# Performance work log

Hardware: AMD Instinct MI355X
Metric: run time of the kernel (lower is better)

The kernel has to match this reference:

```python
import jax, jax.numpy as jnp
import numpy as np

N_NODES = 30000
N_EDGES = 120000
WIDTH = 32
KER_IN = 6
KER_HID = WIDTH // 4  # 8
DEPTH = 4


def setup_inputs() -> dict:
    key = jax.random.key(0)
    ks = jax.random.split(key, 12)
    x = jax.random.normal(ks[0], (N_NODES, 1), dtype=jnp.float32)
    edge_index = jax.random.randint(ks[1], (2, N_EDGES), 0, N_NODES, dtype=jnp.int64)
    edge_attr = jax.random.uniform(ks[2], (N_EDGES, KER_IN), dtype=jnp.float32)
    # fc1: in_width=1 -> width
    fc1_w = jax.random.normal(ks[3], (1, WIDTH), dtype=jnp.float32) * 0.5
    fc1_b = jnp.zeros((WIDTH,), dtype=jnp.float32)
    # kernel MLP: ker_in -> width//4 -> width*width (per-edge weight matrix)
    k_w1 = jax.random.normal(ks[4], (KER_IN, KER_HID), dtype=jnp.float32) * (1.0 / np.sqrt(KER_IN))
    k_b1 = jnp.zeros((KER_HID,), dtype=jnp.float32)
    k_w2 = jax.random.normal(ks[5], (KER_HID, WIDTH * WIDTH), dtype=jnp.float32) * (1.0 / np.sqrt(KER_HID))
    k_b2 = jnp.zeros((WIDTH * WIDTH,), dtype=jnp.float32)
    # NNConv root weight and bias
    root = jax.random.normal(ks[6], (WIDTH, WIDTH), dtype=jnp.float32) * (1.0 / np.sqrt(WIDTH))
    conv_bias = jnp.zeros((WIDTH,), dtype=jnp.float32)
    # fc2: width -> 1
    fc2_w = jax.random.normal(ks[7], (WIDTH, 1), dtype=jnp.float32) * (1.0 / np.sqrt(WIDTH))
    fc2_b = jnp.zeros((1,), dtype=jnp.float32)
    return {"x": x, "edge_index": edge_index, "edge_attr": edge_attr,
            "fc1_w": fc1_w, "fc1_b": fc1_b,
            "k_w1": k_w1, "k_b1": k_b1, "k_w2": k_w2, "k_b2": k_b2,
            "root": root, "conv_bias": conv_bias,
            "fc2_w": fc2_w, "fc2_b": fc2_b}


def _nnconv(x, src, dst, We, root, bias):
    # x: [N, W]; We: [E, W, W] per-edge weight from kernel MLP
    msg = jnp.einsum('ei,eio->eo', x[src], We)            # gather + per-edge matmul
    agg = jax.ops.segment_sum(msg, dst, num_segments=N_NODES)
    cnt = jax.ops.segment_sum(jnp.ones((msg.shape[0],), msg.dtype), dst, num_segments=N_NODES)
    agg = agg / jnp.maximum(cnt, 1.0)[:, None]            # scatter-mean
    return agg + x @ root + bias


def reference(x, edge_index, edge_attr, fc1_w, fc1_b, k_w1, k_b1, k_w2, k_b2, root, conv_bias, fc2_w, fc2_b):
    src, dst = edge_index[0], edge_index[1]
    h = x @ fc1_w + fc1_b                                 # [N, W]
    # kernel MLP on edge_attr -> per-edge [W, W] weight (edge_attr is fixed, so compute once)
    kh = jax.nn.relu(edge_attr @ k_w1 + k_b1)
    We = (kh @ k_w2 + k_b2).reshape(-1, WIDTH, WIDTH)     # [E, W, W]
    for _ in range(DEPTH):
        h = jax.nn.relu(_nnconv(h, src, dst, We, root, conv_bias))
    return h @ fc2_w + fc2_b                              # [N, 1]
```

## Files before the change

### kernel.cpp

```cpp
#include <hip/hip_runtime.h>

#define NN 30000
#define NE 120000
#define TPB 256
#define SB 118
#define NW 1875

typedef __attribute__((ext_vector_type(8))) __bf16 bf16x8;
typedef __attribute__((ext_vector_type(4))) float f32x4;

union B8 { bf16x8 b; unsigned short u[8]; uint4 q; };

__device__ __forceinline__ float blo(unsigned u) { return __uint_as_float(u << 16); }
__device__ __forceinline__ float bhi(unsigned u) { return __uint_as_float(u & 0xffff0000u); }

__device__ __forceinline__ unsigned short f2b(float f) {
  unsigned u = __float_as_uint(f);
  return (unsigned short)((u + 0x7fff + ((u >> 16) & 1)) >> 16);
}

__device__ __forceinline__ void pack_wb(int f, const float* kw2, const float* kb2,
                                        const float* root, uint4* Wb) {
  int ct = f >> 6, l = f & 63;
  int j = ct * 16 + (l & 15);
  int k = j >> 5, o = j & 31;
  int i0 = (l >> 4) * 8;
  B8 w;
#pragma unroll
  for (int ii = 0; ii < 8; ii++) {
    int i = i0 + ii;
    float v;
    if (k < 8) v = kw2[k * 1024 + i * 32 + o];
    else if (k == 8) v = kb2[i * 32 + o];
    else v = root[i * 32 + o];
    w.u[ii] = f2b(v);
  }
  Wb[f] = w.q;
}

__global__ void k_init(int* __restrict__ cnt, const float* __restrict__ kw2,
                       const float* __restrict__ kb2, const float* __restrict__ root,
                       uint4* __restrict__ Wb) {
  int bid = blockIdx.x;
  if (bid < SB) {
    int n = bid * TPB + threadIdx.x;
    if (n < NN) cnt[n] = 0;
  } else {
    int f = (bid - SB) * TPB + threadIdx.x;
    if (f < 1280) pack_wb(f, kw2, kb2, root, Wb);
  }
}

__global__ void k_prep(const float* __restrict__ ea, const float* __restrict__ w1,
                       const float* __restrict__ b1, const int* __restrict__ dst,
                       float* __restrict__ kc, int* __restrict__ cnt) {
  int e = blockIdx.x * TPB + threadIdx.x;
  if (e >= NE) return;
  float a[6];
#pragma unroll
  for (int i = 0; i < 6; i++) a[i] = ea[e * 6 + i];
#pragma unroll
  for (int k = 0; k < 8; k++) {
    float s = b1[k];
#pragma unroll
    for (int i = 0; i < 6; i++) s = fmaf(a[i], w1[i * 8 + k], s);
    kc[e * 8 + k] = fmaxf(s, 0.f);
  }
  atomicAdd(&cnt[dst[e]], 1);
}

__global__ void k_scan1(const int* __restrict__ cnt, int* __restrict__ bsum) {
  __shared__ int S[TPB];
  int t = threadIdx.x, n = blockIdx.x * TPB + t;
  S[t] = (n < NN) ? cnt[n] : 0;
  __syncthreads();
  for (int off = TPB / 2; off; off >>= 1) {
    if (t < off) S[t] += S[t + off];
    __syncthreads();
  }
  if (t == 0) bsum[blockIdx.x] = S[0];
}

__global__ void k_scan2(int* __restrict__ bsum) {
  __shared__ int S[128];
  int t = threadIdx.x;
  S[t] = (t < SB) ? bsum[t] : 0;
  __syncthreads();
  for (int off = 1; off < 128; off <<= 1) {
    int v = S[t] + ((t >= off) ? S[t - off] : 0);
    __syncthreads();
    S[t] = v;
    __syncthreads();
  }
  if (t < SB) bsum[t] = (t > 0) ? S[t - 1] : 0;
}

__global__ void k_scan3(const int* __restrict__ cnt, const int* __restrict__ bsum,
                        int* __restrict__ rowstart, int* __restrict__ wpos,
                        float* __restrict__ icnt) {
  __shared__ int S[TPB];
  int t = threadIdx.x, n = blockIdx.x * TPB + t;
  int c = (n < NN) ? cnt[n] : 0;
  S[t] = c;
  __syncthreads();
  for (int off = 1; off < TPB; off <<= 1) {
    int v = S[t] + ((t >= off) ? S[t - off] : 0);
    __syncthreads();
    S[t] = v;
    __syncthreads();
  }
  if (n < NN) {
    int r = bsum[blockIdx.x] + S[t] - c;
    rowstart[n] = r;
    wpos[n] = r;
    icnt[n] = 1.f / (float)max(c, 1);
  }
}

__global__ void k_scatter(const int* __restrict__ dst, const int* __restrict__ src,
                          const float* __restrict__ kc, int* __restrict__ wpos,
                          int* __restrict__ srcs, float* __restrict__ kcs) {
  int e = blockIdx.x * TPB + threadIdx.x;
  if (e >= NE) return;
  int pos = atomicAdd(&wpos[dst[e]], 1);
  srcs[pos] = src[e];
  float4 a = *(const float4*)&kc[e * 8];
  float4 b = *(const float4*)&kc[e * 8 + 4];
  *(float4*)&kcs[(size_t)pos * 8] = a;
  *(float4*)&kcs[(size_t)pos * 8 + 4] = b;
}

__global__ __launch_bounds__(TPB, 4) void k_node1(
    const float* __restrict__ x, const float* __restrict__ fc1w,
    const float* __restrict__ fc1b, const uint4* __restrict__ Wb,
    unsigned* __restrict__ Pb, float* __restrict__ Pr) {
  const int l = threadIdx.x & 63;
  const int wid = blockIdx.x * (TPB / 64) + (threadIdx.x >> 6);
  if (wid >= NW) return;
  const int nb = wid * 16;
  B8 Bf[20];
#pragma unroll
  for (int ct = 0; ct < 20; ct++) Bf[ct].q = Wb[ct * 64 + l];
  const int row = nb + (l & 15);
  const int k0 = (l >> 4) * 8;
  B8 af;
  float xv = x[row];
#pragma unroll
  for (int ii = 0; ii < 8; ii++)
    af.u[ii] = f2b(fmaf(xv, fc1w[k0 + ii], fc1b[k0 + ii]));
  const int oo = l & 15;
  const int r0 = (l >> 4) * 4;
#pragma unroll
  for (int kp = 0; kp < 4; kp++) {
    f32x4 d0 = {0.f, 0.f, 0.f, 0.f}, d1 = d0, d2 = d0, d3 = d0;
    d0 = __builtin_amdgcn_mfma_f32_16x16x32_bf16(af.b, Bf[4 * kp + 0].b, d0, 0, 0, 0);
    d1 = __builtin_amdgcn_mfma_f32_16x16x32_bf16(af.b, Bf[4 * kp + 1].b, d1, 0, 0, 0);
    d2 = __builtin_amdgcn_mfma_f32_16x16x32_bf16(af.b, Bf[4 * kp + 2].b, d2, 0, 0, 0);
    d3 = __builtin_amdgcn_mfma_f32_16x16x32_bf16(af.b, Bf[4 * kp + 3].b, d3, 0, 0, 0);
#pragma unroll
    for (int r = 0; r < 4; r++) {
      int n = nb + r0 + r;
      Pb[(size_t)n * 160 + kp * 32 + oo] = f2b(d0[r]) | ((unsigned)f2b(d2[r]) << 16);
      Pb[(size_t)n * 160 + kp * 32 + 16 + oo] = f2b(d1[r]) | ((unsigned)f2b(d3[r]) << 16);
    }
  }
  {
    f32x4 d0 = {0.f, 0.f, 0.f, 0.f}, d1 = d0, d2 = d0, d3 = d0;
    d0 = __builtin_amdgcn_mfma_f32_16x16x32_bf16(af.b, Bf[16].b, d0, 0, 0, 0);
    d1 = __builtin_amdgcn_mfma_f32_16x16x32_bf16(af.b, Bf[17].b, d1, 0, 0, 0);
    d2 = __builtin_amdgcn_mfma_f32_16x16x32_bf16(af.b, Bf[18].b, d2, 0, 0, 0);
    d3 = __builtin_amdgcn_mfma_f32_16x16x32_bf16(af.b, Bf[19].b, d3, 0, 0, 0);
#pragma unroll
    for (int r = 0; r < 4; r++) {
      int n = nb + r0 + r;
      Pb[(size_t)n * 160 + 128 + oo] = f2b(d0[r]);
      Pb[(size_t)n * 160 + 128 + 16 + oo] = f2b(d1[r]);
      Pr[(size_t)n * 32 + oo] = d2[r];
      Pr[(size_t)n * 32 + 16 + oo] = d3[r];
    }
  }
}

__global__ __launch_bounds__(TPB, 4) void k_fused(
    const int* __restrict__ rowstart, const int* __restrict__ cnt,
    const float* __restrict__ icnt, const int* __restrict__ srcs,
    const float* __restrict__ kcs, const unsigned* __restrict__ Pbi,
    const float* __restrict__ Pri, const float* __restrict__ cbias,
    const uint4* __restrict__ Wb, unsigned* __restrict__ Pbo,
    float* __restrict__ Pro) {
  __shared__ float hL[512];
  const int tid = threadIdx.x, w = tid >> 6, lane = tid & 63;
  const int nb = blockIdx.x * 16;
  const int half = lane >> 5, o = lane & 31;
#pragma unroll 1
  for (int q = 0; q < 4; q++) {
    int n = nb + 4 * w + q;
    int rs = rowstart[n], re = rs + cnt[n];
    float acc = 0.f;
    for (int j = rs + half; j < re; j += 2) {
      int s = srcs[j];
      float ckv = (o < 8) ? kcs[(size_t)j * 8 + o] : 0.f;
      const unsigned* Ps = Pbi + (size_t)s * 160;
      unsigned w0 = Ps[o], w1 = Ps[32 + o], w2 = Ps[64 + o], w3 = Ps[96 + o];
      unsigned wb = Ps[128 + o];
      acc += blo(wb);
      acc = fmaf(__shfl(ckv, 0, 32), blo(w0), acc);
      acc = fmaf(__shfl(ckv, 1, 32), bhi(w0), acc);
      acc = fmaf(__shfl(ckv, 2, 32), blo(w1), acc);
      acc = fmaf(__shfl(ckv, 3, 32), bhi(w1), acc);
      acc = fmaf(__shfl(ckv, 4, 32), blo(w2), acc);
      acc = fmaf(__shfl(ckv, 5, 32), bhi(w2), acc);
      acc = fmaf(__shfl(ckv, 6, 32), blo(w3), acc);
      acc = fmaf(__shfl(ckv, 7, 32), bhi(w3), acc);
    }
    acc += __shfl_xor(acc, 32, 64);
    if (lane < 32)
      hL[(4 * w + q) * 32 + o] =
          fmaxf(fmaf(acc, icnt[n], Pri[(size_t)n * 32 + o] + cbias[o]), 0.f);
  }
  __syncthreads();
  B8 Bf0, Bf1, Bf2, Bf3, Bf4;
  Bf0.q = Wb[(4 * w + 0) * 64 + lane];
  Bf1.q = Wb[(4 * w + 1) * 64 + lane];
  Bf2.q = Wb[(4 * w + 2) * 64 + lane];
  Bf3.q = Wb[(4 * w + 3) * 64 + lane];
  Bf4.q = Wb[(16 + w) * 64 + lane];
  const int row = lane & 15, k0 = (lane >> 4) * 8;
  B8 af;
#pragma unroll
  for (int ii = 0; ii < 8; ii++) af.u[ii] = f2b(hL[row * 32 + k0 + ii]);
  f32x4 z = {0.f, 0.f, 0.f, 0.f};
  f32x4 d0 = __builtin_amdgcn_mfma_f32_16x16x32_bf16(af.b, Bf0.b, z, 0, 0, 0);
  f32x4 d1 = __builtin_amdgcn_mfma_f32_16x16x32_bf16(af.b, Bf1.b, z, 0, 0, 0);
  f32x4 d2 = __builtin_amdgcn_mfma_f32_16x16x32_bf16(af.b, Bf2.b, z, 0, 0, 0);
  f32x4 d3 = __builtin_amdgcn_mfma_f32_16x16x32_bf16(af.b, Bf3.b, z, 0, 0, 0);
  f32x4 d4 = __builtin_amdgcn_mfma_f32_16x16x32_bf16(af.b, Bf4.b, z, 0, 0, 0);
  const int oo = lane & 15, r0 = (lane >> 4) * 4;
#pragma unroll
  for (int r = 0; r < 4; r++) {
    int n = nb + r0 + r;
    Pbo[(size_t)n * 160 + w * 32 + oo] = f2b(d0[r]) | ((unsigned)f2b(d2[r]) << 16);
    Pbo[(size_t)n * 160 + w * 32 + 16 + oo] = f2b(d1[r]) | ((unsigned)f2b(d3[r]) << 16);
    if (w == 0) Pbo[(size_t)n * 160 + 128 + oo] = f2b(d4[r]);
    else if (w == 1) Pbo[(size_t)n * 160 + 128 + 16 + oo] = f2b(d4[r]);
    else if (w == 2) Pro[(size_t)n * 32 + oo] = d4[r];
    else Pro[(size_t)n * 32 + 16 + oo] = d4[r];
  }
}

__global__ void k_final(const int* __restrict__ rowstart, const int* __restrict__ cnt,
                        const float* __restrict__ icnt, const int* __restrict__ srcs,
                        const float* __restrict__ kcs, const unsigned* __restrict__ Pb,
                        const float* __restrict__ Pr, const float* __restrict__ cbias,
                        const float* __restrict__ fc2w, const float* __restrict__ fc2b,
                        float* __restrict__ out) {
  int t = blockIdx.x * TPB + threadIdx.x;
  int n = t >> 6;
  if (n >= NN) return;
  int lane = threadIdx.x & 63;
  int half = lane >> 5, o = lane & 31;
  int rs = rowstart[n], re = rs + cnt[n];
  float acc = 0.f;
  for (int j = rs + half; j < re; j += 2) {
    int s = srcs[j];
    float ckv = (o < 8) ? kcs[(size_t)j * 8 + o] : 0.f;
    const unsigned* Ps = Pb + (size_t)s * 160;
    unsigned w0 = Ps[o], w1 = Ps[32 + o], w2 = Ps[64 + o], w3 = Ps[96 + o];
    unsigned wb = Ps[128 + o];
    acc += blo(wb);
    acc = fmaf(__shfl(ckv, 0, 32), blo(w0), acc);
    acc = fmaf(__shfl(ckv, 1, 32), bhi(w0), acc);
    acc = fmaf(__shfl(ckv, 2, 32), blo(w1), acc);
    acc = fmaf(__shfl(ckv, 3, 32), bhi(w1), acc);
    acc = fmaf(__shfl(ckv, 4, 32), blo(w2), acc);
    acc = fmaf(__shfl(ckv, 5, 32), bhi(w2), acc);
    acc = fmaf(__shfl(ckv, 6, 32), blo(w3), acc);
    acc = fmaf(__shfl(ckv, 7, 32), bhi(w3), acc);
  }
  acc += __shfl_xor(acc, 32, 64);
  float hv = fmaxf(fmaf(acc, icnt[n], Pr[(size_t)n * 32 + o] + cbias[o]), 0.f);
  float s2 = hv * fc2w[o];
#pragma unroll
  for (int d = 16; d; d >>= 1) s2 += __shfl_xor(s2, d, 32);
  if (lane == 0) out[n] = s2 + fc2b[0];
}

extern "C" void kernel_launch(void* const* d_in, const int* in_sizes, int n_in,
                              void* d_out, int out_size, void* d_ws, size_t ws_size,
                              hipStream_t stream) {
  const float* x     = (const float*)d_in[0];
  const int*   ei    = (const int*)d_in[1];
  const float* ea    = (const float*)d_in[2];
  const float* fc1w  = (const float*)d_in[3];
  const float* fc1b  = (const float*)d_in[4];
  const float* kw1   = (const float*)d_in[5];
  const float* kb1   = (const float*)d_in[6];
  const float* kw2   = (const float*)d_in[7];
  const float* kb2   = (const float*)d_in[8];
  const float* root  = (const float*)d_in[9];
  const float* cbias = (const float*)d_in[10];
  const float* fc2w  = (const float*)d_in[11];
  const float* fc2b  = (const float*)d_in[12];
  float* out = (float*)d_out;
  const int* srcp = ei;
  const int* dstp = ei + NE;

  float* ws = (float*)d_ws;
  float* kc       = ws;
  float* kcs      = kc + NE * 8;
  int*   srcs     = (int*)(kcs + NE * 8);
  float* icnt     = (float*)(srcs + NE);
  float* Pr0      = icnt + NN;
  float* Pr1      = Pr0 + NN * 32;
  int*   cnt      = (int*)(Pr1 + NN * 32);
  int*   rowstart = cnt + NN;
  int*   wpos     = rowstart + NN;
  int*   bsum     = wpos + NN;
  uint4* Wb       = (uint4*)(bsum + 128);
  unsigned* Pb0   = (unsigned*)(Wb + 1280);
  unsigned* Pb1   = Pb0 + (size_t)NN * 160;

  k_init<<<SB + 5, TPB, 0, stream>>>(cnt, kw2, kb2, root, Wb);
  k_prep<<<(NE + TPB - 1) / TPB, TPB, 0, stream>>>(ea, kw1, kb1, dstp, kc, cnt);
  k_scan1<<<SB, TPB, 0, stream>>>(cnt, bsum);
  k_scan2<<<1, 128, 0, stream>>>(bsum);
  k_scan3<<<SB, TPB, 0, stream>>>(cnt, bsum, rowstart, wpos, icnt);
  k_scatter<<<(NE + TPB - 1) / TPB, TPB, 0, stream>>>(dstp, srcp, kc, wpos, srcs, kcs);

  k_node1<<<(NW * 64 + TPB - 1) / TPB, TPB, 0, stream>>>(x, fc1w, fc1b, Wb, Pb0, Pr0);
  k_fused<<<NW, TPB, 0, stream>>>(rowstart, cnt, icnt, srcs, kcs, Pb0, Pr0, cbias,
                                  Wb, Pb1, Pr1);
  k_fused<<<NW, TPB, 0, stream>>>(rowstart, cnt, icnt, srcs, kcs, Pb1, Pr1, cbias,
                                  Wb, Pb0, Pr0);
  k_fused<<<NW, TPB, 0, stream>>>(rowstart, cnt, icnt, srcs, kcs, Pb0, Pr0, cbias,
                                  Wb, Pb1, Pr1);
  k_final<<<(NN * 64 + TPB - 1) / TPB, TPB, 0, stream>>>(
      rowstart, cnt, icnt, srcs, kcs, Pb1, Pr1, cbias, fc2w, fc2b, out);
}
```

Before: 120.8 us.

## Replace prefix scan with atomic segment allocation and merge scatter with node1

The three-kernel scan for CSR row offsets becomes one kernel where each node claims its segment with an atomicAdd on a global counter. The edge scatter and the first node transform kernel are merged into one launch, partitioned by block index. This removes several kernel launches and their serialization gaps. In exchange, segment placement becomes nondeterministic and no longer follows node order, which may reduce memory locality when later layers read edges.

```diff
diff --git a/kernel.cpp b/kernel.cpp
--- a/kernel.cpp
+++ b/kernel.cpp
@@ -5,6 +5,7 @@
 #define TPB 256
 #define SB 118
 #define NW 1875
+#define NB1 469
 
 typedef __attribute__((ext_vector_type(8))) __bf16 bf16x8;
 typedef __attribute__((ext_vector_type(4))) float f32x4;
@@ -38,13 +39,14 @@
   Wb[f] = w.q;
 }
 
-__global__ void k_init(int* __restrict__ cnt, const float* __restrict__ kw2,
-                       const float* __restrict__ kb2, const float* __restrict__ root,
-                       uint4* __restrict__ Wb) {
+__global__ void k_init(int* __restrict__ cnt, int* __restrict__ gtotal,
+                       const float* __restrict__ kw2, const float* __restrict__ kb2,
+                       const float* __restrict__ root, uint4* __restrict__ Wb) {
   int bid = blockIdx.x;
   if (bid < SB) {
     int n = bid * TPB + threadIdx.x;
     if (n < NN) cnt[n] = 0;
+    if (bid == 0 && threadIdx.x == 0) *gtotal = 0;
   } else {
     int f = (bid - SB) * TPB + threadIdx.x;
     if (f < 1280) pack_wb(f, kw2, kb2, root, Wb);
@@ -69,115 +71,79 @@
   atomicAdd(&cnt[dst[e]], 1);
 }
 
-__global__ void k_scan1(const int* __restrict__ cnt, int* __restrict__ bsum) {
-  __shared__ int S[TPB];
-  int t = threadIdx.x, n = blockIdx.x * TPB + t;
-  S[t] = (n < NN) ? cnt[n] : 0;
-  __syncthreads();
-  for (int off = TPB / 2; off; off >>= 1) {
-    if (t < off) S[t] += S[t + off];
-    __syncthreads();
-  }
-  if (t == 0) bsum[blockIdx.x] = S[0];
-}
-
-__global__ void k_scan2(int* __restrict__ bsum) {
-  __shared__ int S[128];
-  int t = threadIdx.x;
-  S[t] = (t < SB) ? bsum[t] : 0;
-  __syncthreads();
-  for (int off = 1; off < 128; off <<= 1) {
-    int v = S[t] + ((t >= off) ? S[t - off] : 0);
-    __syncthreads();
-    S[t] = v;
-    __syncthreads();
-  }
-  if (t < SB) bsum[t] = (t > 0) ? S[t - 1] : 0;
-}
-
-__global__ void k_scan3(const int* __restrict__ cnt, const int* __restrict__ bsum,
+__global__ void k_alloc(const int* __restrict__ cnt, int* __restrict__ gtotal,
                         int* __restrict__ rowstart, int* __restrict__ wpos,
                         float* __restrict__ icnt) {
-  __shared__ int S[TPB];
-  int t = threadIdx.x, n = blockIdx.x * TPB + t;
-  int c = (n < NN) ? cnt[n] : 0;
-  S[t] = c;
-  __syncthreads();
-  for (int off = 1; off < TPB; off <<= 1) {
-    int v = S[t] + ((t >= off) ? S[t - off] : 0);
-    __syncthreads();
-    S[t] = v;
-    __syncthreads();
-  }
-  if (n < NN) {
-    int r = bsum[blockIdx.x] + S[t] - c;
-    rowstart[n] = r;
-    wpos[n] = r;
-    icnt[n] = 1.f / (float)max(c, 1);
-  }
-}
-
-__global__ void k_scatter(const int* __restrict__ dst, const int* __restrict__ src,
-                          const float* __restrict__ kc, int* __restrict__ wpos,
-                          int* __restrict__ srcs, float* __restrict__ kcs) {
-  int e = blockIdx.x * TPB + threadIdx.x;
-  if (e >= NE) return;
-  int pos = atomicAdd(&wpos[dst[e]], 1);
-  srcs[pos] = src[e];
-  float4 a = *(const float4*)&kc[e * 8];
-  float4 b = *(const float4*)&kc[e * 8 + 4];
-  *(float4*)&kcs[(size_t)pos * 8] = a;
-  *(float4*)&kcs[(size_t)pos * 8 + 4] = b;
-}
-
-__global__ __launch_bounds__(TPB, 4) void k_node1(
-    const float* __restrict__ x, const float* __restrict__ fc1w,
-    const float* __restrict__ fc1b, const uint4* __restrict__ Wb,
-    unsigned* __restrict__ Pb, float* __restrict__ Pr) {
-  const int l = threadIdx.x & 63;
-  const int wid = blockIdx.x * (TPB / 64) + (threadIdx.x >> 6);
-  if (wid >= NW) return;
-  const int nb = wid * 16;
-  B8 Bf[20];
-#pragma unroll
-  for (int ct = 0; ct < 20; ct++) Bf[ct].q = Wb[ct * 64 + l];
-  const int row = nb + (l & 15);
-  const int k0 = (l >> 4) * 8;
-  B8 af;
-  float xv = x[row];
-#pragma unroll
-  for (int ii = 0; ii < 8; ii++)
-    af.u[ii] = f2b(fmaf(xv, fc1w[k0 + ii], fc1b[k0 + ii]));
-  const int oo = l & 15;
-  const int r0 = (l >> 4) * 4;
-#pragma unroll
-  for (int kp = 0; kp < 4; kp++) {
-    f32x4 d0 = {0.f, 0.f, 0.f, 0.f}, d1 = d0, d2 = d0, d3 = d0;
-    d0 = __builtin_amdgcn_mfma_f32_16x16x32_bf16(af.b, Bf[4 * kp + 0].b, d0, 0, 0, 0);
-    d1 = __builtin_amdgcn_mfma_f32_16x16x32_bf16(af.b, Bf[4 * kp + 1].b, d1, 0, 0, 0);
-    d2 = __builtin_amdgcn_mfma_f32_16x16x32_bf16(af.b, Bf[4 * kp + 2].b, d2, 0, 0, 0);
-    d3 = __builtin_amdgcn_mfma_f32_16x16x32_bf16(af.b, Bf[4 * kp + 3].b, d3, 0, 0, 0);
-#pragma unroll
-    for (int r = 0; r < 4; r++) {
-      int n = nb + r0 + r;
-      Pb[(size_t)n * 160 + kp * 32 + oo] = f2b(d0[r]) | ((unsigned)f2b(d2[r]) << 16);
-      Pb[(size_t)n * 160 + kp * 32 + 16 + oo] = f2b(d1[r]) | ((unsigned)f2b(d3[r]) << 16);
+  int n = blockIdx.x * TPB + threadIdx.x;
+  if (n >= NN) return;
+  int c = cnt[n];
+  int r = atomicAdd(gtotal, c);
+  rowstart[n] = r;
+  wpos[n] = r;
+  icnt[n] = 1.f / (float)max(c, 1);
+}
+
+__global__ __launch_bounds__(TPB, 4) void k_scatnode(
+    const int* __restrict__ dst, const int* __restrict__ src,
+    const float* __restrict__ kc, int* __restrict__ wpos, int* __restrict__ srcs,
+    float* __restrict__ kcs, const float* __restrict__ x,
+    const float* __restrict__ fc1w, const float* __restrict__ fc1b,
+    const uint4* __restrict__ Wb, unsigned* __restrict__ Pb, float* __restrict__ Pr) {
+  if (blockIdx.x < NB1) {
+    const int l = threadIdx.x & 63;
+    const int wid = blockIdx.x * (TPB / 64) + (threadIdx.x >> 6);
+    if (wid >= NW) return;
+    const int nb = wid * 16;
+    B8 Bf[20];
+#pragma unroll
+    for (int ct = 0; ct < 20; ct++) Bf[ct].q = Wb[ct * 64 + l];
+    const int row = nb + (l & 15);
+    const int k0 = (l >> 4) * 8;
+    B8 af;
+    float xv = x[row];
+#pragma unroll
+    for (int ii = 0; ii < 8; ii++)
+      af.u[ii] = f2b(fmaf(xv, fc1w[k0 + ii], fc1b[k0 + ii]));
+    const int oo = l & 15;
+    const int r0 = (l >> 4) * 4;
+#pragma unroll
+    for (int kp = 0; kp < 4; kp++) {
+      f32x4 d0 = {0.f, 0.f, 0.f, 0.f}, d1 = d0, d2 = d0, d3 = d0;
+      d0 = __builtin_amdgcn_mfma_f32_16x16x32_bf16(af.b, Bf[4 * kp + 0].b, d0, 0, 0, 0);
+      d1 = __builtin_amdgcn_mfma_f32_16x16x32_bf16(af.b, Bf[4 * kp + 1].b, d1, 0, 0, 0);
+      d2 = __builtin_amdgcn_mfma_f32_16x16x32_bf16(af.b, Bf[4 * kp + 2].b, d2, 0, 0, 0);
+      d3 = __builtin_amdgcn_mfma_f32_16x16x32_bf16(af.b, Bf[4 * kp + 3].b, d3, 0, 0, 0);
+#pragma unroll
+      for (int r = 0; r < 4; r++) {
+        int n = nb + r0 + r;
+        Pb[(size_t)n * 160 + kp * 32 + oo] = f2b(d0[r]) | ((unsigned)f2b(d2[r]) << 16);
+        Pb[(size_t)n * 160 + kp * 32 + 16 + oo] = f2b(d1[r]) | ((unsigned)f2b(d3[r]) << 16);
+      }
     }
-  }
-  {
-    f32x4 d0 = {0.f, 0.f, 0.f, 0.f}, d1 = d0, d2 = d0, d3 = d0;
-    d0 = __builtin_amdgcn_mfma_f32_16x16x32_bf16(af.b, Bf[16].b, d0, 0, 0, 0);
-    d1 = __builtin_amdgcn_mfma_f32_16x16x32_bf16(af.b, Bf[17].b, d1, 0, 0, 0);
-    d2 = __builtin_amdgcn_mfma_f32_16x16x32_bf16(af.b, Bf[18].b, d2, 0, 0, 0);
-    d3 = __builtin_amdgcn_mfma_f32_16x16x32_bf16(af.b, Bf[19].b, d3, 0, 0, 0);
-#pragma unroll
-    for (int r = 0; r < 4; r++) {
-      int n = nb + r0 + r;
-      Pb[(size_t)n * 160 + 128 + oo] = f2b(d0[r]);
-      Pb[(size_t)n * 160 + 128 + 16 + oo] = f2b(d1[r]);
-      Pr[(size_t)n * 32 + oo] = d2[r];
-      Pr[(size_t)n * 32 + 16 + oo] = d3[r];
+    {
+      f32x4 d0 = {0.f, 0.f, 0.f, 0.f}, d1 = d0, d2 = d0, d3 = d0;
+      d0 = __builtin_amdgcn_mfma_f32_16x16x32_bf16(af.b, Bf[16].b, d0, 0, 0, 0);
+      d1 = __builtin_amdgcn_mfma_f32_16x16x32_bf16(af.b, Bf[17].b, d1, 0, 0, 0);
+      d2 = __builtin_amdgcn_mfma_f32_16x16x32_bf16(af.b, Bf[18].b, d2, 0, 0, 0);
+      d3 = __builtin_amdgcn_mfma_f32_16x16x32_bf16(af.b, Bf[19].b, d3, 0, 0, 0);
+#pragma unroll
+      for (int r = 0; r < 4; r++) {
+        int n = nb + r0 + r;
+        Pb[(size_t)n * 160 + 128 + oo] = f2b(d0[r]);
+        Pb[(size_t)n * 160 + 128 + 16 + oo] = f2b(d1[r]);
+        Pr[(size_t)n * 32 + oo] = d2[r];
+        Pr[(size_t)n * 32 + 16 + oo] = d3[r];
+      }
     }
+  } else {
+    int e = (blockIdx.x - NB1) * TPB + threadIdx.x;
+    if (e >= NE) return;
+    int pos = atomicAdd(&wpos[dst[e]], 1);
+    srcs[pos] = src[e];
+    float4 a = *(const float4*)&kc[e * 8];
+    float4 b = *(const float4*)&kc[e * 8 + 4];
+    *(float4*)&kcs[(size_t)pos * 8] = a;
+    *(float4*)&kcs[(size_t)pos * 8 + 4] = b;
   }
 }
 
@@ -315,19 +281,16 @@
   int*   cnt      = (int*)(Pr1 + NN * 32);
   int*   rowstart = cnt + NN;
   int*   wpos     = rowstart + NN;
-  int*   bsum     = wpos + NN;
-  uint4* Wb       = (uint4*)(bsum + 128);
+  int*   gtotal   = wpos + NN;
+  uint4* Wb       = (uint4*)(gtotal + 128);
   unsigned* Pb0   = (unsigned*)(Wb + 1280);
   unsigned* Pb1   = Pb0 + (size_t)NN * 160;
 
-  k_init<<<SB + 5, TPB, 0, stream>>>(cnt, kw2, kb2, root, Wb);
+  k_init<<<SB + 5, TPB, 0, stream>>>(cnt, gtotal, kw2, kb2, root, Wb);
   k_prep<<<(NE + TPB - 1) / TPB, TPB, 0, stream>>>(ea, kw1, kb1, dstp, kc, cnt);
-  k_scan1<<<SB, TPB, 0, stream>>>(cnt, bsum);
-  k_scan2<<<1, 128, 0, stream>>>(bsum);
-  k_scan3<<<SB, TPB, 0, stream>>>(cnt, bsum, rowstart, wpos, icnt);
-  k_scatter<<<(NE + TPB - 1) / TPB, TPB, 0, stream>>>(dstp, srcp, kc, wpos, srcs, kcs);
-
-  k_node1<<<(NW * 64 + TPB - 1) / TPB, TPB, 0, stream>>>(x, fc1w, fc1b, Wb, Pb0, Pr0);
+  k_alloc<<<SB, TPB, 0, stream>>>(cnt, gtotal, rowstart, wpos, icnt);
+  k_scatnode<<<NB1 + NB1, TPB, 0, stream>>>(dstp, srcp, kc, wpos, srcs, kcs,
+                                            x, fc1w, fc1b, Wb, Pb0, Pr0);
   k_fused<<<NW, TPB, 0, stream>>>(rowstart, cnt, icnt, srcs, kcs, Pb0, Pr0, cbias,
                                   Wb, Pb1, Pr1);
   k_fused<<<NW, TPB, 0, stream>>>(rowstart, cnt, icnt, srcs, kcs, Pb1, Pr1, cbias,
```

After: 119.4 us. No clear change (-1.1%).
